# Optimization experiments

Measured on AMD Instinct MI355X. Metric: run time of the kernel, lower is better.

The kernel has to match this reference:

```python
import jax, jax.numpy as jnp
import numpy as np

N = 100000   # nodes
E = 3200000  # edges per graph
D = 16       # embedding_size, num_heads = 1
ATTN_SLOPE = 0.2   # DGL GATv2Conv negative_slope default
ACT_SLOPE = 0.01   # torch.nn.functional.leaky_relu default (activation arg)


def gatv2_layer(h, src, dst, W_src, b_src, W_dst, b_dst, attn):
    """DGL GATv2Conv with num_heads=1, activation=leaky_relu.
    h: [N, D]; src/dst: [E] int; W_*: [D, D]; b_*: [D]; attn: [D].
    """
    feat_src = h @ W_src + b_src          # [N, D]
    feat_dst = h @ W_dst + b_dst          # [N, D]
    el = feat_src[src]                    # [E, D] gather to edges
    e = jax.nn.leaky_relu(el + feat_dst[dst], ATTN_SLOPE)  # [E, D]
    score = e @ attn                      # [E] attention logits
    # segment softmax over incoming edges of each destination node
    smax = jax.ops.segment_max(score, dst, num_segments=N)
    smax = jnp.where(jnp.isfinite(smax), smax, 0.0)  # empty segments -> 0
    ex = jnp.exp(score - smax[dst])       # [E]
    denom = jax.ops.segment_sum(ex, dst, num_segments=N)  # [N]
    alpha = ex / denom[dst]               # [E]
    rst = jax.ops.segment_sum(alpha[:, None] * el, dst, num_segments=N)  # [N, D]
    return jax.nn.leaky_relu(rst, ACT_SLOPE)


def setup_inputs() -> dict:
    key = jax.random.key(0)
    ks = jax.random.split(key, 16)
    s = 1.0 / np.sqrt(D)
    return {
        "embedding": jax.random.normal(ks[0], (N, D), jnp.float32),
        "src1": jax.random.randint(ks[1], (E,), 0, N, jnp.int32),
        "dst1": jax.random.randint(ks[2], (E,), 0, N, jnp.int32),
        "src2": jax.random.randint(ks[3], (E,), 0, N, jnp.int32),
        "dst2": jax.random.randint(ks[4], (E,), 0, N, jnp.int32),
        "W_src1": jax.random.normal(ks[5], (D, D), jnp.float32) * s,
        "b_src1": jnp.zeros((D,), jnp.float32),
        "W_dst1": jax.random.normal(ks[6], (D, D), jnp.float32) * s,
        "b_dst1": jnp.zeros((D,), jnp.float32),
        "attn1": jax.random.normal(ks[7], (D,), jnp.float32) * s,
        "W_src2": jax.random.normal(ks[8], (D, D), jnp.float32) * s,
        "b_src2": jnp.zeros((D,), jnp.float32),
        "W_dst2": jax.random.normal(ks[9], (D, D), jnp.float32) * s,
        "b_dst2": jnp.zeros((D,), jnp.float32),
        "attn2": jax.random.normal(ks[10], (D,), jnp.float32) * s,
    }


def reference(embedding, src1, dst1, src2, dst2,
              W_src1, b_src1, W_dst1, b_dst1, attn1,
              W_src2, b_src2, W_dst2, b_dst2, attn2):
    user2item = gatv2_layer(embedding, src1, dst1, W_src1, b_src1, W_dst1, b_dst1, attn1)
    item_influence = gatv2_layer(user2item, src2, dst2, W_src2, b_src2, W_dst2, b_dst2, attn2)
    return item_influence  # [N, D]
```

## Files before the change

kernel.cpp:

```cpp
#include <hip/hip_runtime.h>
#include <hip/hip_fp16.h>

#define D 16
#define R 64
#define RBITS 6
#define RMASK 63
#define STRIDE 2560
#define CAP 2560
#define KPT (CAP / 256)
#define EPB 8192
#define K1T 1024
#define NB2 1664
#define ATTN_SLOPE 0.2f
#define ACT_SLOPE 0.01f

__device__ __forceinline__ float leaky_a(float v) {
    return v > 0.f ? v : ATTN_SLOPE * v;
}
__device__ __forceinline__ float2 h2f(unsigned u) {
    __half2 h = *(__half2*)&u;
    return __half22float2(h);
}


__device__ void binscatter_tile(int tile, const int* __restrict__ src,
                                const int* __restrict__ dst,
                                int* __restrict__ gcur, unsigned* __restrict__ binned,
                                int E, int NB, char* sb) {
    unsigned* sorted = (unsigned*)sb;
    unsigned short* sposb = (unsigned short*)(sb + 32768);
    int* soffs = (int*)(sb + 49152);
    int* delta = (int*)(sb + 49152 + 4 * NB2);
    int* swsum = (int*)(sb + 49152 + 8 * NB2);
    int tid = threadIdx.x;
    int base = tile * EPB;
    int count = E - base;
    if (count > EPB) count = EPB;
    bool full = (count == EPB);

    for (int i = tid; i < NB; i += K1T) soffs[i] = 0;
    __syncthreads();
    int dd[8];
    if (full) {
        const int4* d4 = (const int4*)(dst + base);
        int4 a = d4[tid], b = d4[K1T + tid];
        dd[0] = a.x; dd[1] = a.y; dd[2] = a.z; dd[3] = a.w;
        dd[4] = b.x; dd[5] = b.y; dd[6] = b.z; dd[7] = b.w;
#pragma unroll
        for (int m = 0; m < 8; m++) atomicAdd(&soffs[dd[m] >> RBITS], 1);
    } else {
        for (int k = 0; k < 8; k++) {
            int e = base + k * K1T + tid;
            if (e < E) atomicAdd(&soffs[dst[e] >> RBITS], 1);
        }
    }
    __syncthreads();
    int i0 = 2 * tid, i1 = 2 * tid + 1;
    int a0 = (i0 < NB) ? soffs[i0] : 0;
    int a1 = (i1 < NB) ? soffs[i1] : 0;
    int pair = a0 + a1;
    int lane = tid & 63, w = tid >> 6;
    int x = pair;
#pragma unroll
    for (int ofs = 1; ofs < 64; ofs <<= 1) {
        int y = __shfl_up(x, ofs, 64);
        if (lane >= ofs) x += y;
    }
    if (lane == 63) swsum[w] = x;
    __syncthreads();
    if (w == 0) {
        int v = (lane < 16) ? swsum[lane] : 0;
        int s = v;
#pragma unroll
        for (int ofs = 1; ofs < 16; ofs <<= 1) {
            int y = __shfl_up(s, ofs, 64);
            if (lane >= ofs) s += y;
        }
        if (lane < 16) swsum[lane] = s - v;
    }
    __syncthreads();
    int excl = x - pair + swsum[w];
    __syncthreads();
    if (i0 < NB) {
        soffs[i0] = excl;
        if (a0 > 0) {
            int res = atomicAdd(&gcur[i0], a0);
            delta[i0] = i0 * STRIDE + res - excl;
        }
    }
    if (i1 < NB) {
        soffs[i1] = excl + a0;
        if (a1 > 0) {
            int res = atomicAdd(&gcur[i1], a1);
            delta[i1] = i1 * STRIDE + res - (excl + a0);
        }
    }
    __syncthreads();
    if (full) {
        const int4* s4 = (const int4*)(src + base);
        int4 sa = s4[tid], sb4 = s4[K1T + tid];
        int ss[8] = {sa.x, sa.y, sa.z, sa.w, sb4.x, sb4.y, sb4.z, sb4.w};
#pragma unroll
        for (int m = 0; m < 8; m++) {
            int b = dd[m] >> RBITS;
            int r = atomicAdd(&soffs[b], 1);
            sorted[r] = ((unsigned)ss[m] << RBITS) | (unsigned)(dd[m] & RMASK);
            sposb[r] = (unsigned short)b;
        }
    } else {
        for (int k = 0; k < 8; k++) {
            int e = base + k * K1T + tid;
            if (e < E) {
                int dv = dst[e];
                int b = dv >> RBITS;
                int r = atomicAdd(&soffs[b], 1);
                sorted[r] = ((unsigned)src[e] << RBITS) | (unsigned)(dv & RMASK);
                sposb[r] = (unsigned short)b;
            }
        }
    }
    __syncthreads();
#pragma unroll
    for (int m = 0; m < 8; m++) {
        int p = m * K1T + tid;
        if (p < count) {
            int b = sposb[p];
            int pos = p + delta[b];
            if (pos < (b + 1) * STRIDE) binned[pos] = sorted[p];
        }
    }
}

__device__ void transform_tile(int tile, const float* __restrict__ h,
                               const float* __restrict__ Ws, const float* __restrict__ bs,
                               const float* __restrict__ Wd, const float* __restrict__ bd,
                               __half* __restrict__ fsh, float* __restrict__ fdst,
                               int N, char* sb) {
    float* sWs = (float*)sb;
    float* sWd = sWs + 256;
    float* sbs = sWd + 256;
    float* sbd = sbs + 16;
    int t = threadIdx.x;
    if (t < 256) { sWs[t] = Ws[t]; sWd[t] = Wd[t]; }
    if (t < 16) { sbs[t] = bs[t]; sbd[t] = bd[t]; }
    __syncthreads();
    int n = tile * K1T + t;
    if (n >= N) return;
    float hv[D];
    const float4* h4 = (const float4*)(h + (size_t)n * D);
#pragma unroll
    for (int k = 0; k < 4; k++) {
        float4 v = h4[k];
        hv[4 * k] = v.x; hv[4 * k + 1] = v.y; hv[4 * k + 2] = v.z; hv[4 * k + 3] = v.w;
    }
    float os[D], od[D];
#pragma unroll
    for (int d = 0; d < D; d++) {
        float ss = sbs[d];
        float sd = sbd[d];
#pragma unroll
        for (int k = 0; k < D; k++) {
            ss += hv[k] * sWs[k * D + d];
            sd += hv[k] * sWd[k * D + d];
        }
        os[d] = ss; od[d] = sd;
    }
    unsigned us[8];
#pragma unroll
    for (int k = 0; k < 8; k++) {
        __half2 hh = __floats2half2_rn(os[2 * k], os[2 * k + 1]);
        us[k] = *(unsigned*)&hh;
    }
    uint4* fo = (uint4*)(fsh + (size_t)n * D);
    fo[0] = make_uint4(us[0], us[1], us[2], us[3]);
    fo[1] = make_uint4(us[4], us[5], us[6], us[7]);
    float4* fd4 = (float4*)(fdst + (size_t)n * D);
#pragma unroll
    for (int k = 0; k < 4; k++)
        fd4[k] = make_float4(od[4 * k], od[4 * k + 1], od[4 * k + 2], od[4 * k + 3]);
}

__global__ void __launch_bounds__(K1T)
k1_kernel(const float* h, const float* Ws, const float* bs,
          const float* Wd, const float* bd,
          __half* fsh, float* fdst,
          const int* srcA, const int* dstA, int* gA, unsigned* binnedA, int EA,
          const int* srcB, const int* dstB, int* gB, unsigned* binnedB, int EB,
          int N, int NB, int B1, int B2, int TT) {
    __shared__ __align__(16) char sb[49152 + 8 * NB2 + 64];
    int bid = blockIdx.x;
    if (bid < B1) {
        binscatter_tile(bid, srcA, dstA, gA, binnedA, EA, NB, sb);
    } else if (bid < B1 + B2) {
        binscatter_tile(bid - B1, srcB, dstB, gB, binnedB, EB, NB, sb);
    } else {
        int t = bid - B1 - B2;
        if (t < TT) transform_tile(t, h, Ws, bs, Wd, bd, fsh, fdst, N, sb);
    }
}


template <bool DO_TAIL>
__global__ void __launch_bounds__(256)
acc_kernel(const unsigned* __restrict__ binned, const int* __restrict__ gcur,
           const __half* __restrict__ fsh, const float* __restrict__ fdst,
           const float* __restrict__ attn, float* __restrict__ out,
           __half* __restrict__ fs2h, float* __restrict__ fd2,
           const float* __restrict__ Ws2, const float* __restrict__ bs2,
           const float* __restrict__ Wd2, const float* __restrict__ bd2,
           int N) {
    __shared__ float sfd[R * D];
    __shared__ int ebuf[CAP];
    __shared__ float exbuf[CAP];
    __shared__ int cstart[R + 1];
    __shared__ int cur[R];
    int b = blockIdx.x;
    int tid = threadIdx.x;
    int node0 = b * R;
    int nn = N - node0;
    if (nn > R) nn = R;
    for (int i = tid; i < nn * D; i += 256) sfd[i] = fdst[node0 * D + i];
    if (tid <= R) cstart[tid] = 0;

    float av[D];
#pragma unroll
    for (int k = 0; k < D; k++) av[k] = attn[k];

    int cnt = gcur[b];
    if (cnt > CAP) cnt = CAP;
    int base = b * STRIDE;

    unsigned pls[KPT];
#pragma unroll
    for (int k = 0; k < KPT; k++) {
        int j = k * 256 + tid;
        pls[k] = (j < cnt) ? binned[base + j] : 0xFFFFFFFFu;
    }
    __syncthreads();

    const uint4* fsh4 = (const uint4*)fsh;
    const uint2* fsq = (const uint2*)fsh;
    const float4* sfd4 = (const float4*)sfd;

#pragma unroll
    for (int k = 0; k < KPT; k++)
        if (pls[k] != 0xFFFFFFFFu) atomicAdd(&cstart[pls[k] & RMASK], 1);

    float exs[KPT];
#pragma unroll
    for (int k = 0; k < KPT; k += 2) {
        unsigned q0 = pls[k], q1 = pls[k + 1];
        uint4 ua0, ub0, ua1, ub1;
        if (q0 != 0xFFFFFFFFu) {
            int s = q0 >> RBITS;
            ua0 = fsh4[2 * s]; ub0 = fsh4[2 * s + 1];
        }
        if (q1 != 0xFFFFFFFFu) {
            int s = q1 >> RBITS;
            ua1 = fsh4[2 * s]; ub1 = fsh4[2 * s + 1];
        }
        if (q0 != 0xFFFFFFFFu) {
            int loc = q0 & RMASK;
            float4 f0 = sfd4[loc * 4 + 0], f1 = sfd4[loc * 4 + 1];
            float4 f2 = sfd4[loc * 4 + 2], f3 = sfd4[loc * 4 + 3];
            float2 c0 = h2f(ua0.x), c1 = h2f(ua0.y), c2 = h2f(ua0.z), c3 = h2f(ua0.w);
            float2 c4 = h2f(ub0.x), c5 = h2f(ub0.y), c6 = h2f(ub0.z), c7 = h2f(ub0.w);
            float p = leaky_a(c0.x + f0.x) * av[0]  + leaky_a(c0.y + f0.y) * av[1]
                    + leaky_a(c1.x + f0.z) * av[2]  + leaky_a(c1.y + f0.w) * av[3]
                    + leaky_a(c2.x + f1.x) * av[4]  + leaky_a(c2.y + f1.y) * av[5]
                    + leaky_a(c3.x + f1.z) * av[6]  + leaky_a(c3.y + f1.w) * av[7]
                    + leaky_a(c4.x + f2.x) * av[8]  + leaky_a(c4.y + f2.y) * av[9]
                    + leaky_a(c5.x + f2.z) * av[10] + leaky_a(c5.y + f2.w) * av[11]
                    + leaky_a(c6.x + f3.x) * av[12] + leaky_a(c6.y + f3.y) * av[13]
                    + leaky_a(c7.x + f3.z) * av[14] + leaky_a(c7.y + f3.w) * av[15];
            exs[k] = __expf(p);
        }
        if (q1 != 0xFFFFFFFFu) {
            int loc = q1 & RMASK;
            float4 f0 = sfd4[loc * 4 + 0], f1 = sfd4[loc * 4 + 1];
            float4 f2 = sfd4[loc * 4 + 2], f3 = sfd4[loc * 4 + 3];
            float2 c0 = h2f(ua1.x), c1 = h2f(ua1.y), c2 = h2f(ua1.z), c3 = h2f(ua1.w);
            float2 c4 = h2f(ub1.x), c5 = h2f(ub1.y), c6 = h2f(ub1.z), c7 = h2f(ub1.w);
            float p = leaky_a(c0.x + f0.x) * av[0]  + leaky_a(c0.y + f0.y) * av[1]
                    + leaky_a(c1.x + f0.z) * av[2]  + leaky_a(c1.y + f0.w) * av[3]
                    + leaky_a(c2.x + f1.x) * av[4]  + leaky_a(c2.y + f1.y) * av[5]
                    + leaky_a(c3.x + f1.z) * av[6]  + leaky_a(c3.y + f1.w) * av[7]
                    + leaky_a(c4.x + f2.x) * av[8]  + leaky_a(c4.y + f2.y) * av[9]
                    + leaky_a(c5.x + f2.z) * av[10] + leaky_a(c5.y + f2.w) * av[11]
                    + leaky_a(c6.x + f3.x) * av[12] + leaky_a(c6.y + f3.y) * av[13]
                    + leaky_a(c7.x + f3.z) * av[14] + leaky_a(c7.y + f3.w) * av[15];
            exs[k + 1] = __expf(p);
        }
    }
    __syncthreads();
    if (tid < R) {
        int v = cstart[tid];
        int x = v;
#pragma unroll
        for (int ofs = 1; ofs < 64; ofs <<= 1) {
            int y = __shfl_up(x, ofs, 64);
            if (tid >= ofs) x += y;
        }
        cstart[tid] = x - v;
        cur[tid] = x - v;
        if (tid == R - 1) cstart[R] = x;
    }
    __syncthreads();
#pragma unroll
    for (int k = 0; k < KPT; k++) {
        unsigned pl = pls[k];
        if (pl != 0xFFFFFFFFu) {
            int r = atomicAdd(&cur[pl & RMASK], 1);
            ebuf[r] = (int)pl;
            exbuf[r] = exs[k];
        }
    }
    __syncthreads();

    int lane = tid & 63;
    int w = tid >> 6;
    int q = lane & 3;
    int s2 = (lane >> 2) & 3;
    int n2 = lane >> 4;

    float4 acc[4];
    float den[4];
#pragma unroll
    for (int i = 0; i < 4; i++) {
        acc[i] = make_float4(0.f, 0.f, 0.f, 0.f);
        den[i] = 0.f;
    }
#pragma unroll
    for (int i = 0; i < 4; i++) {
        int loc = w * 16 + i * 4 + n2;
        int kb = cstart[loc], ke = cstart[loc + 1];
        int k = kb + s2;
        for (; k + 12 < ke; k += 16) {
            int pl0 = ebuf[k];
            int pl1 = ebuf[k + 4];
            int pl2 = ebuf[k + 8];
            int pl3 = ebuf[k + 12];
            float ex0 = exbuf[k];
            float ex1 = exbuf[k + 4];
            float ex2 = exbuf[k + 8];
            float ex3 = exbuf[k + 12];
            uint2 u0 = fsq[(((unsigned)pl0) >> RBITS) * 4 + q];
            uint2 u1 = fsq[(((unsigned)pl1) >> RBITS) * 4 + q];
            uint2 u2 = fsq[(((unsigned)pl2) >> RBITS) * 4 + q];
            uint2 u3 = fsq[(((unsigned)pl3) >> RBITS) * 4 + q];
            float2 a01 = h2f(u0.x), a23 = h2f(u0.y);
            float2 b01 = h2f(u1.x), b23 = h2f(u1.y);
            float2 c01 = h2f(u2.x), c23 = h2f(u2.y);
            float2 d01 = h2f(u3.x), d23 = h2f(u3.y);
            acc[i].x += ex0 * a01.x + ex1 * b01.x + ex2 * c01.x + ex3 * d01.x;
            acc[i].y += ex0 * a01.y + ex1 * b01.y + ex2 * c01.y + ex3 * d01.y;
            acc[i].z += ex0 * a23.x + ex1 * b23.x + ex2 * c23.x + ex3 * d23.x;
            acc[i].w += ex0 * a23.y + ex1 * b23.y + ex2 * c23.y + ex3 * d23.y;
            den[i] += (ex0 + ex1) + (ex2 + ex3);
        }
        for (; k < ke; k += 4) {
            int pl = ebuf[k];
            float ex = exbuf[k];
            uint2 u = fsq[(((unsigned)pl) >> RBITS) * 4 + q];
            float2 a01 = h2f(u.x), a23 = h2f(u.y);
            acc[i].x += ex * a01.x;
            acc[i].y += ex * a01.y;
            acc[i].z += ex * a23.x;
            acc[i].w += ex * a23.y;
            den[i] += ex;
        }
    }
#pragma unroll
    for (int i = 0; i < 4; i++) {
        float4 a = acc[i];
        float dn = den[i];
#pragma unroll
        for (int m = 4; m <= 8; m <<= 1) {
            a.x += __shfl_xor(a.x, m, 16);
            a.y += __shfl_xor(a.y, m, 16);
            a.z += __shfl_xor(a.z, m, 16);
            a.w += __shfl_xor(a.w, m, 16);
            dn += __shfl_xor(dn, m, 16);
        }
        int loc = w * 16 + i * 4 + n2;
        if (s2 == 0 && loc < nn) {
            float inv = dn > 0.f ? 1.f / dn : 0.f;
            float4 v;
            v.x = a.x * inv; v.x = v.x > 0.f ? v.x : ACT_SLOPE * v.x;
            v.y = a.y * inv; v.y = v.y > 0.f ? v.y : ACT_SLOPE * v.y;
            v.z = a.z * inv; v.z = v.z > 0.f ? v.z : ACT_SLOPE * v.z;
            v.w = a.w * inv; v.w = v.w > 0.f ? v.w : ACT_SLOPE * v.w;
            if (DO_TAIL) {
                *(float4*)&sfd[loc * D + q * 4] = v;
            } else {
                ((float4*)out)[(size_t)(node0 + loc) * 4 + q] = v;
            }
        }
    }
    if (DO_TAIL) {
        __syncthreads();
        float* wb = (float*)ebuf;
        if (tid < 256) { wb[tid] = Ws2[tid]; wb[256 + tid] = Wd2[tid]; }
        if (tid < 16) { wb[512 + tid] = bs2[tid]; wb[528 + tid] = bd2[tid]; }
        __syncthreads();
        int loc = tid >> 2, qq = tid & 3;
        if (loc < nn) {
            float hvv[16];
#pragma unroll
            for (int k = 0; k < 16; k++) hvv[k] = sfd[loc * D + k];
            float s0 = wb[512 + 4 * qq], s1 = wb[513 + 4 * qq];
            float s2v = wb[514 + 4 * qq], s3 = wb[515 + 4 * qq];
            float d0 = wb[528 + 4 * qq], d1 = wb[529 + 4 * qq];
            float d2v = wb[530 + 4 * qq], d3 = wb[531 + 4 * qq];
#pragma unroll
            for (int k = 0; k < 16; k++) {
                float hk = hvv[k];
                const float* wr = &wb[k * 16 + 4 * qq];
                const float* wr2 = &wb[256 + k * 16 + 4 * qq];
                s0 += hk * wr[0]; s1 += hk * wr[1]; s2v += hk * wr[2]; s3 += hk * wr[3];
                d0 += hk * wr2[0]; d1 += hk * wr2[1]; d2v += hk * wr2[2]; d3 += hk * wr2[3];
            }
            __half2 p0 = __floats2half2_rn(s0, s1), p1 = __floats2half2_rn(s2v, s3);
            *(uint2*)(fs2h + (size_t)(node0 + loc) * D + 4 * qq) =
                make_uint2(*(unsigned*)&p0, *(unsigned*)&p1);
            *(float4*)(fd2 + (size_t)(node0 + loc) * D + 4 * qq) =
                make_float4(d0, d1, d2v, d3);
        }
    }
}


extern "C" void kernel_launch(void* const* d_in, const int* in_sizes, int n_in,
                              void* d_out, int out_size, void* d_ws, size_t ws_size,
                              hipStream_t stream) {
    const float* emb = (const float*)d_in[0];
    const int* src1 = (const int*)d_in[1];
    const int* dst1 = (const int*)d_in[2];
    const int* src2 = (const int*)d_in[3];
    const int* dst2 = (const int*)d_in[4];
    const float* Wsrc1 = (const float*)d_in[5];
    const float* bsrc1 = (const float*)d_in[6];
    const float* Wdst1 = (const float*)d_in[7];
    const float* bdst1 = (const float*)d_in[8];
    const float* attn1 = (const float*)d_in[9];
    const float* Wsrc2 = (const float*)d_in[10];
    const float* bsrc2 = (const float*)d_in[11];
    const float* Wdst2 = (const float*)d_in[12];
    const float* bdst2 = (const float*)d_in[13];
    const float* attn2 = (const float*)d_in[14];

    const int N = in_sizes[0] / D;
    const int E1 = in_sizes[1];
    const int E2 = in_sizes[3];
    const int NB = (N + R - 1) / R;
    const size_t ndf = (size_t)N * D;

    float* ws = (float*)d_ws;
    float* fd1 = ws;
    float* fd2 = fd1 + ndf;
    __half* fs1h = (__half*)(fd2 + ndf);
    __half* fs2h = fs1h + ndf;
    int* gA = (int*)(fs2h + ndf);
    int* gB = gA + NB2;
    unsigned* binned1 = (unsigned*)(gB + NB2);
    unsigned* binned2big = binned1 + (size_t)NB * STRIDE;
    size_t bigNeed = (size_t)((char*)(binned2big + (size_t)NB * STRIDE) - (char*)d_ws);
    bool big = ws_size >= bigNeed;
    (void)n_in; (void)out_size;

    const int B1 = (E1 + EPB - 1) / EPB;
    const int B2 = (E2 + EPB - 1) / EPB;
    const int TT = (N + K1T - 1) / K1T;

    (void)hipMemsetAsync(gA, 0, 2 * NB2 * sizeof(int), stream);

    if (big) {
        k1_kernel<<<B1 + B2 + TT, K1T, 0, stream>>>(
            emb, Wsrc1, bsrc1, Wdst1, bdst1, fs1h, fd1,
            src1, dst1, gA, binned1, E1,
            src2, dst2, gB, binned2big, E2,
            N, NB, B1, B2, TT);
        acc_kernel<true><<<NB, 256, 0, stream>>>(
            binned1, gA, fs1h, fd1, attn1, nullptr,
            fs2h, fd2, Wsrc2, bsrc2, Wdst2, bdst2, N);
        acc_kernel<false><<<NB, 256, 0, stream>>>(
            binned2big, gB, fs2h, fd2, attn2, (float*)d_out,
            nullptr, nullptr, nullptr, nullptr, nullptr, nullptr, N);
    } else {
        k1_kernel<<<B1 + TT, K1T, 0, stream>>>(
            emb, Wsrc1, bsrc1, Wdst1, bdst1, fs1h, fd1,
            src1, dst1, gA, binned1, E1,
            src2, dst2, gB, binned1, 0,
            N, NB, B1, 0, TT);
        acc_kernel<true><<<NB, 256, 0, stream>>>(
            binned1, gA, fs1h, fd1, attn1, nullptr,
            fs2h, fd2, Wsrc2, bsrc2, Wdst2, bdst2, N);
        k1_kernel<<<B2, K1T, 0, stream>>>(
            emb, Wsrc1, bsrc1, Wdst1, bdst1, fs1h, fd1,
            src2, dst2, gB, binned1, E2,
            src2, dst2, gB, binned1, 0,
            N, NB, B2, 0, 0);
        acc_kernel<false><<<NB, 256, 0, stream>>>(
            binned1, gB, fs2h, fd2, attn2, (float*)d_out,
            nullptr, nullptr, nullptr, nullptr, nullptr, nullptr, N);
    }
}
```

Before: 241.7 us.

## Halve binning tile size and double accumulation block threads

Binscatter tiles drop from 8192 to 4096 edges with 512 threads, so shared memory per block halves and more blocks can be resident. The prefix scan is restructured so each thread handles 4 bins, with a serial sum over wave totals. The accumulation kernel now uses 512 threads per 64-node bin, with 2 node groups per wave instead of 4 and an odd-KPT tail path. Layer-2 weights are staged in a dedicated shared buffer at kernel start. This adds more global atomics on the bin counters and more shared memory in the accumulation kernel.

```diff
diff --git a/kernel.cpp b/kernel.cpp
--- a/kernel.cpp
+++ b/kernel.cpp
@@ -7,9 +7,10 @@
 #define RMASK 63
 #define STRIDE 2560
 #define CAP 2560
-#define KPT (CAP / 256)
-#define EPB 8192
-#define K1T 1024
+#define ACCT 512
+#define KPT (CAP / ACCT)
+#define EPB2 4096
+#define K1T 512
 #define NB2 1664
 #define ATTN_SLOPE 0.2f
 #define ACT_SLOPE 0.01f
@@ -28,15 +29,15 @@
                                 int* __restrict__ gcur, unsigned* __restrict__ binned,
                                 int E, int NB, char* sb) {
     unsigned* sorted = (unsigned*)sb;
-    unsigned short* sposb = (unsigned short*)(sb + 32768);
-    int* soffs = (int*)(sb + 49152);
-    int* delta = (int*)(sb + 49152 + 4 * NB2);
-    int* swsum = (int*)(sb + 49152 + 8 * NB2);
+    unsigned short* sposb = (unsigned short*)(sb + 16384);
+    int* soffs = (int*)(sb + 24576);
+    int* delta = (int*)(sb + 24576 + 4 * NB2);
+    int* swsum = (int*)(sb + 24576 + 8 * NB2);
     int tid = threadIdx.x;
-    int base = tile * EPB;
+    int base = tile * EPB2;
     int count = E - base;
-    if (count > EPB) count = EPB;
-    bool full = (count == EPB);
+    if (count > EPB2) count = EPB2;
+    bool full = (count == EPB2);
 
     for (int i = tid; i < NB; i += K1T) soffs[i] = 0;
     __syncthreads();
@@ -55,12 +56,16 @@
         }
     }
     __syncthreads();
-    int i0 = 2 * tid, i1 = 2 * tid + 1;
-    int a0 = (i0 < NB) ? soffs[i0] : 0;
-    int a1 = (i1 < NB) ? soffs[i1] : 0;
-    int pair = a0 + a1;
+    int c[4];
+    int tsum = 0;
+#pragma unroll
+    for (int m = 0; m < 4; m++) {
+        int i = tid * 4 + m;
+        c[m] = (i < NB) ? soffs[i] : 0;
+        tsum += c[m];
+    }
     int lane = tid & 63, w = tid >> 6;
-    int x = pair;
+    int x = tsum;
 #pragma unroll
     for (int ofs = 1; ofs < 64; ofs <<= 1) {
         int y = __shfl_up(x, ofs, 64);
@@ -68,31 +73,19 @@
     }
     if (lane == 63) swsum[w] = x;
     __syncthreads();
-    if (w == 0) {
-        int v = (lane < 16) ? swsum[lane] : 0;
-        int s = v;
-#pragma unroll
-        for (int ofs = 1; ofs < 16; ofs <<= 1) {
-            int y = __shfl_up(s, ofs, 64);
-            if (lane >= ofs) s += y;
-        }
-        if (lane < 16) swsum[lane] = s - v;
-    }
-    __syncthreads();
-    int excl = x - pair + swsum[w];
-    __syncthreads();
-    if (i0 < NB) {
-        soffs[i0] = excl;
-        if (a0 > 0) {
-            int res = atomicAdd(&gcur[i0], a0);
-            delta[i0] = i0 * STRIDE + res - excl;
-        }
-    }
-    if (i1 < NB) {
-        soffs[i1] = excl + a0;
-        if (a1 > 0) {
-            int res = atomicAdd(&gcur[i1], a1);
-            delta[i1] = i1 * STRIDE + res - (excl + a0);
+    int wofs = 0;
+    for (int j = 0; j < w; j++) wofs += swsum[j];
+    int run = x - tsum + wofs;
+#pragma unroll
+    for (int m = 0; m < 4; m++) {
+        int i = tid * 4 + m;
+        if (i < NB) {
+            soffs[i] = run;
+            if (c[m] > 0) {
+                int res = atomicAdd(&gcur[i], c[m]);
+                delta[i] = i * STRIDE + res - run;
+            }
+            run += c[m];
         }
     }
     __syncthreads();
@@ -187,7 +180,7 @@
           const int* srcA, const int* dstA, int* gA, unsigned* binnedA, int EA,
           const int* srcB, const int* dstB, int* gB, unsigned* binnedB, int EB,
           int N, int NB, int B1, int B2, int TT) {
-    __shared__ __align__(16) char sb[49152 + 8 * NB2 + 64];
+    __shared__ __align__(16) char sb[24576 + 8 * NB2 + 32];
     int bid = blockIdx.x;
     if (bid < B1) {
         binscatter_tile(bid, srcA, dstA, gA, binnedA, EA, NB, sb);
@@ -201,7 +194,7 @@
 
 
 template <bool DO_TAIL>
-__global__ void __launch_bounds__(256)
+__global__ void __launch_bounds__(ACCT)
 acc_kernel(const unsigned* __restrict__ binned, const int* __restrict__ gcur,
            const __half* __restrict__ fsh, const float* __restrict__ fdst,
            const float* __restrict__ attn, float* __restrict__ out,
@@ -214,13 +207,18 @@
     __shared__ float exbuf[CAP];
     __shared__ int cstart[R + 1];
     __shared__ int cur[R];
+    __shared__ float wtail[544];
     int b = blockIdx.x;
     int tid = threadIdx.x;
     int node0 = b * R;
     int nn = N - node0;
     if (nn > R) nn = R;
-    for (int i = tid; i < nn * D; i += 256) sfd[i] = fdst[node0 * D + i];
+    for (int i = tid; i < nn * D; i += ACCT) sfd[i] = fdst[node0 * D + i];
     if (tid <= R) cstart[tid] = 0;
+    if (DO_TAIL) {
+        if (tid < 256) { wtail[tid] = Ws2[tid]; wtail[256 + tid] = Wd2[tid]; }
+        if (tid < 16) { wtail[512 + tid] = bs2[tid]; wtail[528 + tid] = bd2[tid]; }
+    }
 
     float av[D];
 #pragma unroll
@@ -233,7 +231,7 @@
     unsigned pls[KPT];
 #pragma unroll
     for (int k = 0; k < KPT; k++) {
-        int j = k * 256 + tid;
+        int j = k * ACCT + tid;
         pls[k] = (j < cnt) ? binned[base + j] : 0xFFFFFFFFu;
     }
     __syncthreads();
@@ -248,7 +246,7 @@
 
     float exs[KPT];
 #pragma unroll
-    for (int k = 0; k < KPT; k += 2) {
+    for (int k = 0; k + 1 < KPT; k += 2) {
         unsigned q0 = pls[k], q1 = pls[k + 1];
         uint4 ua0, ub0, ua1, ub1;
         if (q0 != 0xFFFFFFFFu) {
@@ -292,6 +290,27 @@
             exs[k + 1] = __expf(p);
         }
     }
+    if (KPT & 1) {
+        unsigned q0 = pls[KPT - 1];
+        if (q0 != 0xFFFFFFFFu) {
+            int s = q0 >> RBITS;
+            uint4 ua0 = fsh4[2 * s], ub0 = fsh4[2 * s + 1];
+            int loc = q0 & RMASK;
+            float4 f0 = sfd4[loc * 4 + 0], f1 = sfd4[loc * 4 + 1];
+            float4 f2 = sfd4[loc * 4 + 2], f3 = sfd4[loc * 4 + 3];
+            float2 c0 = h2f(ua0.x), c1 = h2f(ua0.y), c2 = h2f(ua0.z), c3 = h2f(ua0.w);
+            float2 c4 = h2f(ub0.x), c5 = h2f(ub0.y), c6 = h2f(ub0.z), c7 = h2f(ub0.w);
+            float p = leaky_a(c0.x + f0.x) * av[0]  + leaky_a(c0.y + f0.y) * av[1]
+                    + leaky_a(c1.x + f0.z) * av[2]  + leaky_a(c1.y + f0.w) * av[3]
+                    + leaky_a(c2.x + f1.x) * av[4]  + leaky_a(c2.y + f1.y) * av[5]
+                    + leaky_a(c3.x + f1.z) * av[6]  + leaky_a(c3.y + f1.w) * av[7]
+                    + leaky_a(c4.x + f2.x) * av[8]  + leaky_a(c4.y + f2.y) * av[9]
+                    + leaky_a(c5.x + f2.z) * av[10] + leaky_a(c5.y + f2.w) * av[11]
+                    + leaky_a(c6.x + f3.x) * av[12] + leaky_a(c6.y + f3.y) * av[13]
+                    + leaky_a(c7.x + f3.z) * av[14] + leaky_a(c7.y + f3.w) * av[15];
+            exs[KPT - 1] = __expf(p);
+        }
+    }
     __syncthreads();
     if (tid < R) {
         int v = cstart[tid];
@@ -323,16 +342,16 @@
     int s2 = (lane >> 2) & 3;
     int n2 = lane >> 4;
 
-    float4 acc[4];
-    float den[4];
-#pragma unroll
-    for (int i = 0; i < 4; i++) {
+    float4 acc[2];
+    float den[2];
+#pragma unroll
+    for (int i = 0; i < 2; i++) {
         acc[i] = make_float4(0.f, 0.f, 0.f, 0.f);
         den[i] = 0.f;
     }
 #pragma unroll
-    for (int i = 0; i < 4; i++) {
-        int loc = w * 16 + i * 4 + n2;
+    for (int i = 0; i < 2; i++) {
+        int loc = w * 8 + i * 4 + n2;
         int kb = cstart[loc], ke = cstart[loc + 1];
         int k = kb + s2;
         for (; k + 12 < ke; k += 16) {
@@ -371,7 +390,7 @@
         }
     }
 #pragma unroll
-    for (int i = 0; i < 4; i++) {
+    for (int i = 0; i < 2; i++) {
         float4 a = acc[i];
         float dn = den[i];
 #pragma unroll
@@ -382,7 +401,7 @@
             a.w += __shfl_xor(a.w, m, 16);
             dn += __shfl_xor(dn, m, 16);
         }
-        int loc = w * 16 + i * 4 + n2;
+        int loc = w * 8 + i * 4 + n2;
         if (s2 == 0 && loc < nn) {
             float inv = dn > 0.f ? 1.f / dn : 0.f;
             float4 v;
@@ -399,24 +418,20 @@
     }
     if (DO_TAIL) {
         __syncthreads();
-        float* wb = (float*)ebuf;
-        if (tid < 256) { wb[tid] = Ws2[tid]; wb[256 + tid] = Wd2[tid]; }
-        if (tid < 16) { wb[512 + tid] = bs2[tid]; wb[528 + tid] = bd2[tid]; }
-        __syncthreads();
         int loc = tid >> 2, qq = tid & 3;
-        if (loc < nn) {
+        if (tid < 256 && loc < nn) {
             float hvv[16];
 #pragma unroll
             for (int k = 0; k < 16; k++) hvv[k] = sfd[loc * D + k];
-            float s0 = wb[512 + 4 * qq], s1 = wb[513 + 4 * qq];
-            float s2v = wb[514 + 4 * qq], s3 = wb[515 + 4 * qq];
-            float d0 = wb[528 + 4 * qq], d1 = wb[529 + 4 * qq];
-            float d2v = wb[530 + 4 * qq], d3 = wb[531 + 4 * qq];
+            float s0 = wtail[512 + 4 * qq], s1 = wtail[513 + 4 * qq];
+            float s2v = wtail[514 + 4 * qq], s3 = wtail[515 + 4 * qq];
+            float d0 = wtail[528 + 4 * qq], d1 = wtail[529 + 4 * qq];
+            float d2v = wtail[530 + 4 * qq], d3 = wtail[531 + 4 * qq];
 #pragma unroll
             for (int k = 0; k < 16; k++) {
                 float hk = hvv[k];
-                const float* wr = &wb[k * 16 + 4 * qq];
-                const float* wr2 = &wb[256 + k * 16 + 4 * qq];
+                const float* wr = &wtail[k * 16 + 4 * qq];
+                const float* wr2 = &wtail[256 + k * 16 + 4 * qq];
                 s0 += hk * wr[0]; s1 += hk * wr[1]; s2v += hk * wr[2]; s3 += hk * wr[3];
                 d0 += hk * wr2[0]; d1 += hk * wr2[1]; d2v += hk * wr2[2]; d3 += hk * wr2[3];
             }
@@ -468,8 +483,8 @@
     bool big = ws_size >= bigNeed;
     (void)n_in; (void)out_size;
 
-    const int B1 = (E1 + EPB - 1) / EPB;
-    const int B2 = (E2 + EPB - 1) / EPB;
+    const int B1 = (E1 + EPB2 - 1) / EPB2;
+    const int B2 = (E2 + EPB2 - 1) / EPB2;
     const int TT = (N + K1T - 1) / K1T;
 
     (void)hipMemsetAsync(gA, 0, 2 * NB2 * sizeof(int), stream);
@@ -480,10 +495,10 @@
             src1, dst1, gA, binned1, E1,
             src2, dst2, gB, binned2big, E2,
             N, NB, B1, B2, TT);
-        acc_kernel<true><<<NB, 256, 0, stream>>>(
+        acc_kernel<true><<<NB, ACCT, 0, stream>>>(
             binned1, gA, fs1h, fd1, attn1, nullptr,
             fs2h, fd2, Wsrc2, bsrc2, Wdst2, bdst2, N);
-        acc_kernel<false><<<NB, 256, 0, stream>>>(
+        acc_kernel<false><<<NB, ACCT, 0, stream>>>(
             binned2big, gB, fs2h, fd2, attn2, (float*)d_out,
             nullptr, nullptr, nullptr, nullptr, nullptr, nullptr, N);
     } else {
@@ -492,7 +507,7 @@
             src1, dst1, gA, binned1, E1,
             src2, dst2, gB, binned1, 0,
             N, NB, B1, 0, TT);
-        acc_kernel<true><<<NB, 256, 0, stream>>>(
+        acc_kernel<true><<<NB, ACCT, 0, stream>>>(
             binned1, gA, fs1h, fd1, attn1, nullptr,
             fs2h, fd2, Wsrc2, bsrc2, Wdst2, bdst2, N);
         k1_kernel<<<B2, K1T, 0, stream>>>(
@@ -500,7 +515,7 @@
             src2, dst2, gB, binned1, E2,
             src2, dst2, gB, binned1, 0,
             N, NB, B2, 0, 0);
-        acc_kernel<false><<<NB, 256, 0, stream>>>(
+        acc_kernel<false><<<NB, ACCT, 0, stream>>>(
             binned1, gB, fs2h, fd2, attn2, (float*)d_out,
             nullptr, nullptr, nullptr, nullptr, nullptr, nullptr, N);
     }
```

Result: slower. 306.9 us (+27.0%).
